# Performance work log

Measured on AMD Instinct MI355X. Metric: run time of the kernel, lower is better.

The kernel has to match this reference:

```python
import jax, jax.numpy as jnp
import numpy as np

HEADS = 8
DIM_HEAD = 128
SCALE = DIM_HEAD ** -0.5
EPS = 1e-5


def layer_norm(t, w, b):
    mu = t.mean(-1, keepdims=True)
    var = ((t - mu) ** 2).mean(-1, keepdims=True)
    return (t - mu) * jax.lax.rsqrt(var + EPS) * w + b


def setup_inputs() -> dict:
    key = jax.random.key(0)
    ks = jax.random.split(key, 8)
    b, n, dim = 4, 1024, 1024
    inner = HEADS * DIM_HEAD  # 1024
    w = 0.02
    return {
        "x": jax.random.normal(ks[0], (b, n, dim), jnp.float32),
        "cond_info": jax.random.normal(ks[1], (b, n, dim), jnp.float32),
        "ref": jax.random.normal(ks[2], (b, n, dim), jnp.float32),
        "ln_w": jnp.ones((dim,), jnp.float32),
        "ln_b": jnp.zeros((dim,), jnp.float32),
        "cln_w": jnp.ones((dim,), jnp.float32),
        "cln_b": jnp.zeros((dim,), jnp.float32),
        "Wk": jax.random.normal(ks[3], (3 * dim, inner), jnp.float32) * w,
        "Wv": jax.random.normal(ks[4], (2 * dim, inner), jnp.float32) * w,
        "Wo": jax.random.normal(ks[5], (inner, dim), jnp.float32) * w,
        "bo": jnp.zeros((dim,), jnp.float32),
        "th_w": jax.random.normal(ks[6], (HEADS, HEADS), jnp.float32) * 0.3,
        "cth_w": jax.random.normal(ks[7], (HEADS, HEADS), jnp.float32) * 0.3,
    }


def reference(x, cond_info, ref, ln_w, ln_b, cln_w, cln_b, Wk, Wv, Wo, bo, th_w, cth_w):
    b, n, _ = x.shape
    h, d = HEADS, DIM_HEAD
    xn = layer_norm(x, ln_w, ln_b)
    rn = layer_norm(ref, ln_w, ln_b)
    cn = layer_norm(cond_info, cln_w, cln_b)
    # projections (y_to_q output is unused in the original forward; omitted)
    cond = jnp.concatenate([xn, cn, rn], axis=-1) @ Wk   # [b, n, h*d]
    refv = jnp.concatenate([xn, rn], axis=-1) @ Wv       # [b, n, h*d]
    split = lambda t: t.reshape(b, n, h, d).transpose(0, 2, 1, 3)  # b h n d
    cond, refv = split(cond), split(refv)
    sim = jnp.einsum('bhid,bhjd->bhij', cond, refv) * SCALE
    attn = jax.nn.softmax(sim, axis=-1)           # row softmax
    context_attn = jax.nn.softmax(sim, axis=-2)   # column softmax
    # talking heads: 1x1 conv over head dim, weight [out_h, in_h]
    attn = jnp.einsum('gh,bhij->bgij', th_w, attn)
    context_attn = jnp.einsum('gh,bhij->bgij', cth_w, context_attn)
    out = jnp.einsum('bhij,bhjd->bhid', attn, refv)
    context_out = jnp.einsum('bhji,bhjd->bhid', context_attn, cond)
    merge = lambda t: t.transpose(0, 2, 1, 3).reshape(b, n, h * d)
    out = merge(out) @ Wo + bo
    context_out = merge(context_out)
    return out, context_out
```

## Files before the change

### kernel.cpp

```cpp
#include <hip/hip_runtime.h>
#include <hip/hip_bf16.h>
#include <stdint.h>

typedef unsigned short u16;
typedef __attribute__((ext_vector_type(8))) short bf16x8;
typedef __attribute__((ext_vector_type(4))) float f32x4;

#define HEADS 8
#define DHEAD 128
#define NSEQ 1024
#define BATCH 4
#define DIM 1024
#define ATT_SCALE 0.088388347648318447f

static __device__ __forceinline__ float bf2f(u16 u){
  union { unsigned int i; float f; } c; c.i = ((unsigned int)u) << 16; return c.f;
}
static __device__ __forceinline__ u16 f2bf(float f){
  union { float f; unsigned int i; } c; c.f = f;
  unsigned int x = c.i;
  return (u16)((x + 0x7fffu + ((x >> 16) & 1u)) >> 16);
}

static __device__ __forceinline__ void gload_lds16(const void* g, void* l){
  __builtin_amdgcn_global_load_lds((__attribute__((address_space(1))) void*)(g),
                                   (__attribute__((address_space(3))) void*)(l),
                                   16, 0, 0);
}

__global__ __launch_bounds__(256)
void ln3_kernel(const float* __restrict__ x, const float* __restrict__ ref,
                const float* __restrict__ cinfo,
                const float* __restrict__ ln_w, const float* __restrict__ ln_b,
                const float* __restrict__ cln_w, const float* __restrict__ cln_b,
                u16* __restrict__ xn, u16* __restrict__ rn, u16* __restrict__ cn)
{
  const int z = blockIdx.y;
  const float* src = (z==0) ? x : (z==1) ? ref : cinfo;
  const float* w   = (z==2) ? cln_w : ln_w;
  const float* b   = (z==2) ? cln_b : ln_b;
  u16* out         = (z==0) ? xn : (z==1) ? rn : cn;

  const int row = blockIdx.x;
  const int t = threadIdx.x;
  const float* xr = src + (size_t)row * DIM;
  float4 v4 = *(const float4*)(xr + t*4);
  float v[4] = {v4.x, v4.y, v4.z, v4.w};
  float s = v[0]+v[1]+v[2]+v[3];
  __shared__ float red[256];
  red[t] = s; __syncthreads();
  for (int o=128;o;o>>=1){ if (t<o) red[t]+=red[t+o]; __syncthreads(); }
  const float mean = red[0] * (1.0f/DIM);
  __syncthreads();
  s = 0.f;
#pragma unroll
  for (int i=0;i<4;i++){ float d = v[i]-mean; s += d*d; }
  red[t] = s; __syncthreads();
  for (int o=128;o;o>>=1){ if (t<o) red[t]+=red[t+o]; __syncthreads(); }
  const float rstd = rsqrtf(red[0]*(1.0f/DIM) + 1e-5f);
  float4 w4 = *(const float4*)(w + t*4);
  float4 b4 = *(const float4*)(b + t*4);
  float wv[4] = {w4.x, w4.y, w4.z, w4.w};
  float bv[4] = {b4.x, b4.y, b4.z, b4.w};
  union { uint2 u; u16 s[4]; } ov;
#pragma unroll
  for (int i=0;i<4;i++)
    ov.s[i] = f2bf((v[i]-mean)*rstd*wv[i] + bv[i]);
  *(uint2*)(out + (size_t)row*DIM + t*4) = ov.u;
}

__global__ __launch_bounds__(256)
void wcvt_kernel(const float* __restrict__ Wk, const float* __restrict__ Wv,
                 const float* __restrict__ Wo,
                 u16* __restrict__ WkT, u16* __restrict__ WvT, u16* __restrict__ WoT)
{
  const int z = blockIdx.z;
  const int K = (z==0) ? 3072 : (z==1) ? 2048 : 1024;
  if ((int)blockIdx.x*32 >= K) return;
  const float* W = (z==0) ? Wk : (z==1) ? Wv : Wo;
  u16* WT = (z==0) ? WkT : (z==1) ? WvT : WoT;
  __shared__ float tile[32][33];
  const int k0 = blockIdx.x*32, n0 = blockIdx.y*32;
  const int t = threadIdx.x, tc = t&31, tr = t>>5;
#pragma unroll
  for (int p=0;p<4;p++)
    tile[tr+p*8][tc] = W[(size_t)(k0+tr+p*8)*DIM + n0+tc];
  __syncthreads();
#pragma unroll
  for (int p=0;p<4;p++)
    WT[(size_t)(n0+tr+p*8)*K + k0+tc] = f2bf(tile[tc][tr+p*8]);
}

__global__ __launch_bounds__(256)
void gemm_kernel(const u16* __restrict__ A0, const u16* __restrict__ A1,
                 const u16* __restrict__ A2, const u16* __restrict__ A0b,
                 const u16* __restrict__ A1b,
                 const u16* __restrict__ B1, const u16* __restrict__ B2,
                 void* __restrict__ Cv, void* __restrict__ Cv2,
                 const float* __restrict__ bias,
                 int K1, int K2, int lda, int ldb1, int ldb2, int ldc,
                 long a_plane, long b_plane, long c_plane,
                 int epi1, int epi2, int z_split, float alpha)
{
  __shared__ __attribute__((aligned(16))) u16 sA[2][4096];
  __shared__ __attribute__((aligned(16))) u16 sB[2][4096];
  const int t = threadIdx.x;
  const int m0 = blockIdx.y*128, n0 = blockIdx.x*128;
  const int zz = blockIdx.z;
  const bool side = (zz >= z_split);
  const int z = side ? (zz - z_split) : zz;
  const u16* a0 = (side ? A0b : A0) + (size_t)z*a_plane;
  const u16* a1 = (side ? A1b : A1) + (size_t)z*a_plane;
  const u16* a2 = A2 + (size_t)z*a_plane;
  const u16* bB = (side ? B2 : B1) + (size_t)z*b_plane;
  void* Cp = side ? Cv2 : Cv;
  const int EPI = side ? epi2 : epi1;
  const int K   = side ? K2 : K1;
  const int ldb = side ? ldb2 : ldb1;

  const int wave = t>>6, lane = t&63;
  const int wm = (wave>>1)*64, wn = (wave&1)*64;
  const int lm = lane&15, q = lane>>4;

  const f32x4 zero4 = {0.f,0.f,0.f,0.f};
  f32x4 acc[4][4];
#pragma unroll
  for (int i=0;i<4;i++)
#pragma unroll
    for (int j=0;j<4;j++) acc[i][j] = zero4;

  const int arowblk = wave*32;

  const int KT = K >> 5;

  auto issueA = [&](int kt, int buf){
    const int kg = kt<<5, seg = kg>>10, ka = kg&1023;
    const u16* Ap = (seg==0) ? a0 : (seg==1 ? a1 : a2);
#pragma unroll
    for (int rr=0; rr<2; ++rr){
      const int rb = arowblk + rr*16;
      gload_lds16(Ap + (size_t)(m0+rb+lm)*lda + (ka + q*8), &sA[buf][rb*32]);
    }
  };
  auto issueB = [&](int kt, int buf){
    const int kg = kt<<5;
#pragma unroll
    for (int rr=0; rr<2; ++rr){
      const int rb = arowblk + rr*16;
      gload_lds16(bB + (size_t)(n0+rb+lm)*ldb + (kg + q*8), &sB[buf][rb*32]);
    }
  };

  issueA(0, 0);
  issueB(0, 0);

  int cur = 0;
  for (int kt=0; kt<KT; ++kt){
    __syncthreads();
    if (kt+1 < KT){
      issueA(kt+1, cur^1);
      issueB(kt+1, cur^1);
    }
    bf16x8 af[4], bfr[4];
#pragma unroll
    for (int f=0; f<4; ++f){
      af[f]  = *(const bf16x8*)&sA[cur][((wm>>4)+f)*512 + lane*8];
      bfr[f] = *(const bf16x8*)&sB[cur][((wn>>4)+f)*512 + lane*8];
    }
#pragma unroll
    for (int fm=0; fm<4; ++fm)
#pragma unroll
      for (int fn=0; fn<4; ++fn)
        acc[fm][fn] = __builtin_amdgcn_mfma_f32_16x16x32_bf16(af[fm], bfr[fn], acc[fm][fn], 0, 0, 0);
    cur ^= 1;
  }

#pragma unroll
  for (int fm=0; fm<4; ++fm){
#pragma unroll
    for (int fn=0; fn<4; ++fn){
#pragma unroll
      for (int r=0; r<4; ++r){
        const int m = m0 + wm + fm*16 + q*4 + r;
        const int n = n0 + wn + fn*16 + lm;
        float val = acc[fm][fn][r] * alpha;
        if (EPI == 0){
          ((u16*)Cp)[(size_t)z*c_plane + (size_t)m*ldc + n] = f2bf(val);
        } else if (EPI == 1){
          ((u16*)Cp)[((size_t)(z>>3)*NSEQ + m)*DIM + (size_t)(z&7)*DHEAD + n] = f2bf(val);
        } else if (EPI == 2){
          ((float*)Cp)[(size_t)m*ldc + n] = val + bias[n];
        } else if (EPI == 3){
          ((u16*)Cp)[(size_t)(((m>>10)*HEADS + (n>>7))*NSEQ + (m&1023))*DHEAD + (n&127)] = f2bf(val);
        } else {
          ((float*)Cp)[((size_t)(z>>3)*NSEQ + m)*DIM + (size_t)(z&7)*DHEAD + n] = val;
        }
      }
    }
  }
}

__global__ __launch_bounds__(256)
void transpose2_kernel(const u16* __restrict__ cond, const u16* __restrict__ refv,
                       u16* __restrict__ condT, u16* __restrict__ refvT)
{
  __shared__ u16 tile[32][33];
  const int zz = blockIdx.z;
  const u16* X = (zz < 32) ? cond : refv;
  u16* XT      = (zz < 32) ? condT : refvT;
  const int z = zz & 31;
  const int i0 = blockIdx.y*32, d0 = blockIdx.x*32;
  const int t = threadIdx.x;
  const int tc = t & 31, tr = t >> 5;
  const u16* Xp = X + (size_t)z*NSEQ*DHEAD;
#pragma unroll
  for (int p=0;p<4;p++){
    int i = tr + p*8;
    tile[i][tc] = Xp[(size_t)(i0+i)*DHEAD + d0 + tc];
  }
  __syncthreads();
  u16* Op = XT + (size_t)z*DHEAD*NSEQ;
#pragma unroll
  for (int p=0;p<4;p++){
    int d = tr + p*8;
    Op[(size_t)(d0+d)*NSEQ + i0 + tc] = tile[tc][d];
  }
}

__global__ __launch_bounds__(256)
void stats_kernel(const u16* __restrict__ sim,
                  float* __restrict__ rmax, float* __restrict__ rrcp,
                  float* __restrict__ cmax, float* __restrict__ crcp)
{
  __shared__ float smx[4][64], ssm[4][64];
  if (blockIdx.x < 8192){
    const int wave = threadIdx.x >> 6, lane = threadIdx.x & 63;
    const int row = blockIdx.x*4 + wave;
    const u16* sr = sim + (size_t)row * NSEQ;
    float v[16]; float m = -1e30f;
#pragma unroll
    for (int c=0;c<16;c++){ v[c] = bf2f(sr[lane + c*64]); m = fmaxf(m, v[c]); }
#pragma unroll
    for (int off=32; off; off>>=1) m = fmaxf(m, __shfl_xor(m, off));
    float s = 0.f;
#pragma unroll
    for (int c=0;c<16;c++) s += __expf(v[c]-m);
#pragma unroll
    for (int off=32; off; off>>=1) s += __shfl_xor(s, off);
    if (lane == 0){ rmax[row] = m; rrcp[row] = 1.0f/s; }
  } else {
    const int t = threadIdx.x;
    const int jl = t & 63, slice = t >> 6;
    const int c = (blockIdx.x - 8192)*64 + jl;
    const int bh = c >> 10, j = c & 1023;
    const u16* sp = sim + (size_t)bh*NSEQ*NSEQ + j + (size_t)(slice*256)*NSEQ;
    float m0=-1e30f, m1=-1e30f, m2=-1e30f, m3=-1e30f;
    for (int i=0;i<256;i+=4){
      m0 = fmaxf(m0, bf2f(sp[(size_t)(i  )*NSEQ]));
      m1 = fmaxf(m1, bf2f(sp[(size_t)(i+1)*NSEQ]));
      m2 = fmaxf(m2, bf2f(sp[(size_t)(i+2)*NSEQ]));
      m3 = fmaxf(m3, bf2f(sp[(size_t)(i+3)*NSEQ]));
    }
    smx[slice][jl] = fmaxf(fmaxf(m0,m1), fmaxf(m2,m3));
    __syncthreads();
    const float M = fmaxf(fmaxf(smx[0][jl], smx[1][jl]),
                          fmaxf(smx[2][jl], smx[3][jl]));
    float s0=0.f, s1=0.f, s2=0.f, s3=0.f;
    for (int i=0;i<256;i+=4){
      s0 += __expf(bf2f(sp[(size_t)(i  )*NSEQ]) - M);
      s1 += __expf(bf2f(sp[(size_t)(i+1)*NSEQ]) - M);
      s2 += __expf(bf2f(sp[(size_t)(i+2)*NSEQ]) - M);
      s3 += __expf(bf2f(sp[(size_t)(i+3)*NSEQ]) - M);
    }
    ssm[slice][jl] = s0+s1+s2+s3;
    __syncthreads();
    if (slice == 0){
      float S = ssm[0][jl] + ssm[1][jl] + ssm[2][jl] + ssm[3][jl];
      cmax[c] = M; crcp[c] = 1.0f/S;
    }
  }
}

__global__ __launch_bounds__(256)
void mix_kernel(u16* simam,
                const float* __restrict__ rmax, const float* __restrict__ rrcp,
                const float* __restrict__ cmax, const float* __restrict__ crcp,
                const float* __restrict__ thw, const float* __restrict__ cthw,
                u16* __restrict__ cmT)
{
  __shared__ float s_th[64], s_cth[64];
  __shared__ u16 s_cm[8][32][33];
  const int t = threadIdx.x;
  if (t < 64){ s_th[t] = thw[t]; s_cth[t] = cthw[t]; }
  __syncthreads();
  const int b = blockIdx.z, i0 = blockIdx.y*32, j0 = blockIdx.x*32;
  const int tj = t & 31, ti = t >> 5;
  for (int p=0;p<4;p++){
    const int i = ti + p*8;
    float a[8], c[8];
#pragma unroll
    for (int h=0;h<8;h++){
      const int bh = b*8 + h;
      const float v = bf2f(simam[((size_t)bh*NSEQ + (i0+i))*NSEQ + j0 + tj]);
      a[h] = __expf(v - rmax[(size_t)bh*NSEQ + i0+i]) * rrcp[(size_t)bh*NSEQ + i0+i];
      c[h] = __expf(v - cmax[(size_t)bh*NSEQ + j0+tj]) * crcp[(size_t)bh*NSEQ + j0+tj];
    }
#pragma unroll
    for (int g=0;g<8;g++){
      float sa = 0.f, sc = 0.f;
#pragma unroll
      for (int h=0;h<8;h++){ sa += s_th[g*8+h]*a[h]; sc += s_cth[g*8+h]*c[h]; }
      simam[((size_t)(b*8+g)*NSEQ + (i0+i))*NSEQ + j0 + tj] = f2bf(sa);
      s_cm[g][i][tj] = f2bf(sc);
    }
  }
  __syncthreads();
#pragma unroll
  for (int g=0;g<8;g++){
#pragma unroll
    for (int p=0;p<4;p++){
      const int j = ti + p*8;
      cmT[((size_t)(b*8+g)*NSEQ + (j0+j))*NSEQ + i0 + tj] = s_cm[g][tj][j];
    }
  }
}

extern "C" void kernel_launch(void* const* d_in, const int* in_sizes, int n_in,
                              void* d_out, int out_size, void* d_ws, size_t ws_size,
                              hipStream_t stream)
{
  const float* x     = (const float*)d_in[0];
  const float* cinfo = (const float*)d_in[1];
  const float* ref   = (const float*)d_in[2];
  const float* ln_w  = (const float*)d_in[3];
  const float* ln_b  = (const float*)d_in[4];
  const float* cln_w = (const float*)d_in[5];
  const float* cln_b = (const float*)d_in[6];
  const float* Wk    = (const float*)d_in[7];
  const float* Wv    = (const float*)d_in[8];
  const float* Wo    = (const float*)d_in[9];
  const float* bo    = (const float*)d_in[10];
  const float* thw   = (const float*)d_in[11];
  const float* cthw  = (const float*)d_in[12];
  float* out = (float*)d_out;

  char* ws = (char*)d_ws;
  u16* xn    = (u16*)(ws + 0);
  u16* cn    = (u16*)(ws + 8388608);
  u16* rn    = (u16*)(ws + 16777216);
  u16* cond  = (u16*)(ws + 25165824);
  u16* refv  = (u16*)(ws + 33554432);
  u16* condT = (u16*)(ws + 41943040);
  u16* refvT = (u16*)(ws + 50331648);
  u16* sim   = (u16*)(ws + 58720256);
  u16* cmT   = (u16*)(ws + 125829120);
  u16* WkT   = (u16*)(ws + 192937984);
  u16* WvT   = (u16*)(ws + 199229440);
  u16* WoT   = (u16*)(ws + 203423744);
  float* rmax = (float*)(ws + 8388608);
  float* rrcp = (float*)(ws + 8388608 + 131072);
  float* cmax = (float*)(ws + 8388608 + 262144);
  float* crcp = (float*)(ws + 8388608 + 393216);
  u16* out_pre = (u16*)(ws + 0);

  ln3_kernel<<<dim3(4096,3), 256, 0, stream>>>(x, ref, cinfo, ln_w, ln_b,
                                               cln_w, cln_b, xn, rn, cn);

  wcvt_kernel<<<dim3(96,32,3), 256, 0, stream>>>(Wk, Wv, Wo, WkT, WvT, WoT);

  gemm_kernel<<<dim3(8,32,2), 256, 0, stream>>>(
      xn, cn, rn, xn, rn, WkT, WvT, cond, refv, nullptr,
      3072, 2048, DIM, 3072, 2048, 0, 0, 0, 0, 3, 3, 1, 1.0f);

  transpose2_kernel<<<dim3(4,32,64), 256, 0, stream>>>(cond, refv, condT, refvT);

  gemm_kernel<<<dim3(8,8,32), 256, 0, stream>>>(
      cond, cond, cond, cond, cond, refv, refv, sim, sim, nullptr,
      DHEAD, DHEAD, DHEAD, DHEAD, DHEAD, NSEQ,
      (long)NSEQ*DHEAD, (long)NSEQ*DHEAD, (long)NSEQ*NSEQ, 0, 0, 1000000, ATT_SCALE);

  stats_kernel<<<8704, 256, 0, stream>>>(sim, rmax, rrcp, cmax, crcp);

  mix_kernel<<<dim3(32,32,4), 256, 0, stream>>>(sim, rmax, rrcp, cmax, crcp, thw, cthw, cmT);

  gemm_kernel<<<dim3(1,8,64), 256, 0, stream>>>(
      sim, sim, sim, cmT, cmT, refvT, condT, out_pre, out + (size_t)BATCH*NSEQ*DIM, nullptr,
      1024, 1024, NSEQ, NSEQ, NSEQ, 0,
      (long)NSEQ*NSEQ, (long)DHEAD*NSEQ, 0, 1, 4, 32, 1.0f);

  gemm_kernel<<<dim3(8,32,1), 256, 0, stream>>>(
      out_pre, out_pre, out_pre, out_pre, out_pre, WoT, WoT, out, out, bo,
      1024, 1024, DIM, 1024, 1024, DIM, 0, 0, 0, 2, 2, 1000000, 1.0f);
}
```

Before: 469.7 us.

## Split-K the output projection GEMM with a separate bias-add reduction

Replaces the final Wo projection GEMM (256 tiles) with a split-K version that has 4 K-slices and 1024 blocks. Each block writes fp32 partials into the reused sim buffer, and a second kernel sums the slices and adds the bias. The goal is to fill more CUs on a GEMM that otherwise launches too few blocks for the device. In exchange it adds 64MB of partial writes and reads plus an extra launch.

```diff
diff --git a/kernel.cpp b/kernel.cpp
--- a/kernel.cpp
+++ b/kernel.cpp
@@ -198,6 +198,108 @@
       }
     }
   }
+}
+
+__global__ __launch_bounds__(256)
+void gemm8_kernel(const u16* __restrict__ A, const u16* __restrict__ B,
+                  float* __restrict__ P)
+{
+  __shared__ __attribute__((aligned(16))) u16 sA[2][4096];
+  __shared__ __attribute__((aligned(16))) u16 sB[2][4096];
+  const int t = threadIdx.x;
+  const int bid = blockIdx.x;
+  const int w = (bid & 7)*128 + (bid >> 3);
+  const int x = w & 7;
+  const int y = (w >> 3) & 31;
+  const int s = w >> 8;
+  const int m0 = y*128, n0 = x*128, k0 = s*256;
+
+  const int wave = t>>6, lane = t&63;
+  const int wm = (wave>>1)*64, wn = (wave&1)*64;
+  const int lm = lane&15, q = lane>>4;
+
+  const f32x4 zero4 = {0.f,0.f,0.f,0.f};
+  f32x4 acc[4][4];
+#pragma unroll
+  for (int i=0;i<4;i++)
+#pragma unroll
+    for (int j=0;j<4;j++) acc[i][j] = zero4;
+
+  const int arowblk = wave*32;
+
+  auto issueA = [&](int kt, int buf){
+    const int kg = k0 + (kt<<5);
+#pragma unroll
+    for (int rr=0; rr<2; ++rr){
+      const int rb = arowblk + rr*16;
+      gload_lds16(A + (size_t)(m0+rb+lm)*1024 + (kg + q*8), &sA[buf][rb*32]);
+    }
+  };
+  auto issueB = [&](int kt, int buf){
+    const int kg = k0 + (kt<<5);
+#pragma unroll
+    for (int rr=0; rr<2; ++rr){
+      const int rb = arowblk + rr*16;
+      gload_lds16(B + (size_t)(n0+rb+lm)*1024 + (kg + q*8), &sB[buf][rb*32]);
+    }
+  };
+
+  issueA(0, 0);
+  issueB(0, 0);
+
+  int cur = 0;
+  for (int kt=0; kt<8; ++kt){
+    __syncthreads();
+    if (kt+1 < 8){
+      issueA(kt+1, cur^1);
+      issueB(kt+1, cur^1);
+    }
+    bf16x8 af[4], bfr[4];
+#pragma unroll
+    for (int f=0; f<4; ++f){
+      af[f]  = *(const bf16x8*)&sA[cur][((wm>>4)+f)*512 + lane*8];
+      bfr[f] = *(const bf16x8*)&sB[cur][((wn>>4)+f)*512 + lane*8];
+    }
+#pragma unroll
+    for (int fm=0; fm<4; ++fm)
+#pragma unroll
+      for (int fn=0; fn<4; ++fn)
+        acc[fm][fn] = __builtin_amdgcn_mfma_f32_16x16x32_bf16(af[fm], bfr[fn], acc[fm][fn], 0, 0, 0);
+    cur ^= 1;
+  }
+
+  float* Pp = P + (size_t)s*4194304;
+#pragma unroll
+  for (int fm=0; fm<4; ++fm){
+#pragma unroll
+    for (int fn=0; fn<4; ++fn){
+#pragma unroll
+      for (int r=0; r<4; ++r){
+        const int m = m0 + wm + fm*16 + q*4 + r;
+        const int n = n0 + wn + fn*16 + lm;
+        Pp[(size_t)m*1024 + n] = acc[fm][fn][r];
+      }
+    }
+  }
+}
+
+__global__ __launch_bounds__(256)
+void red8_kernel(const float* __restrict__ P, const float* __restrict__ bias,
+                 float* __restrict__ out)
+{
+  const int idx = blockIdx.x*256 + threadIdx.x;
+  const float4* P4 = (const float4*)P;
+  float4 a = P4[idx];
+  float4 b = P4[idx + 1048576];
+  float4 c = P4[idx + 2097152];
+  float4 d = P4[idx + 3145728];
+  float4 bb = ((const float4*)bias)[idx & 255];
+  float4 o;
+  o.x = a.x + b.x + c.x + d.x + bb.x;
+  o.y = a.y + b.y + c.y + d.y + bb.y;
+  o.z = a.z + b.z + c.z + d.z + bb.z;
+  o.w = a.w + b.w + c.w + d.w + bb.w;
+  ((float4*)out)[idx] = o;
 }
 
 __global__ __launch_bounds__(256)
@@ -388,7 +490,6 @@
       1024, 1024, NSEQ, NSEQ, NSEQ, 0,
       (long)NSEQ*NSEQ, (long)DHEAD*NSEQ, 0, 1, 4, 32, 1.0f);
 
-  gemm_kernel<<<dim3(8,32,1), 256, 0, stream>>>(
-      out_pre, out_pre, out_pre, out_pre, out_pre, WoT, WoT, out, out, bo,
-      1024, 1024, DIM, 1024, 1024, DIM, 0, 0, 0, 2, 2, 1000000, 1.0f);
-}
+  gemm8_kernel<<<1024, 256, 0, stream>>>(out_pre, WoT, (float*)sim);
+  red8_kernel<<<4096, 256, 0, stream>>>((const float*)sim, bo, out);
+}
```

Measured after the change: 469.8 us. Within noise of the previous version (+0.0%).
